# Kernel optimization log

Measured on AMD Instinct MI355X. Metric: run time of the kernel, lower is better.

Reference implementation:

```python
import jax, jax.numpy as jnp
import numpy as np

N_NODES = 30000
N_EDGES = 480000
N_GRAPHS = 128
CONV_PARAMS = [[32, 32], [32, 32], [64, 64], [64, 64], [128, 128], [128, 128]]
IN_FEAT = 5
NUM_CENTROID = 100
NUM_CLASS = 2
BN_EPS = 1e-5


def setup_inputs() -> dict:
    key = jax.random.key(0)
    ks = jax.random.split(key, 64)
    inp = {}
    inp['features'] = jax.random.normal(ks[0], (N_NODES, IN_FEAT), jnp.float32)
    inp['src'] = jax.random.randint(ks[1], (N_EDGES,), 0, N_NODES, jnp.int32)
    inp['dst'] = jax.random.randint(ks[2], (N_EDGES,), 0, N_NODES, jnp.int32)
    inp['graph_id'] = jnp.sort(jax.random.randint(ks[3], (N_NODES,), 0, N_GRAPHS, jnp.int32))
    inp['bn_gamma'] = jnp.ones((IN_FEAT,), jnp.float32)
    inp['bn_beta'] = jnp.zeros((IN_FEAT,), jnp.float32)
    in_f = IN_FEAT
    ki = 4
    for i, (c1, c2) in enumerate(CONV_PARAMS):
        # EdgeConv MLP operates on concat([x_i, x_j - x_i]) -> 2*in_f inputs
        s1 = 1.0 / np.sqrt(2 * in_f)
        s2 = 1.0 / np.sqrt(c1)
        inp[f'W1_{i}'] = jax.random.normal(ks[ki], (2 * in_f, c1), jnp.float32) * s1
        inp[f'b1_{i}'] = jnp.zeros((c1,), jnp.float32)
        inp[f'W2_{i}'] = jax.random.normal(ks[ki + 1], (c1, c2), jnp.float32) * s2
        inp[f'b2_{i}'] = jnp.zeros((c2,), jnp.float32)
        ki += 2
        in_f = c2
    inp['centroids'] = jax.random.normal(ks[ki], (NUM_CENTROID, CONV_PARAMS[-1][-1]), jnp.float32)
    inp['fc_w'] = jax.random.normal(ks[ki + 1], (NUM_CENTROID, NUM_CLASS), jnp.float32) * (1.0 / np.sqrt(NUM_CENTROID))
    inp['fc_b'] = jnp.zeros((NUM_CLASS,), jnp.float32)
    return inp


def _edge_conv(x, src, dst, deg_inv, W1, b1, W2, b2):
    # DGCNN-style EdgeConv: MLP([x_i, x_j - x_i]) then mean-aggregate to dst node
    xi = x[dst]                                   # [E, F]
    xj = x[src]                                   # [E, F]
    e = jnp.concatenate([xi, xj - xi], axis=-1)   # [E, 2F]
    h = jax.nn.relu(e @ W1 + b1)
    h = jax.nn.relu(h @ W2 + b2)
    return jax.ops.segment_sum(h, dst, num_segments=x.shape[0]) * deg_inv


def reference(features, src, dst, graph_id, bn_gamma, bn_beta,
              W1_0, b1_0, W2_0, b2_0, W1_1, b1_1, W2_1, b2_1,
              W1_2, b1_2, W2_2, b2_2, W1_3, b1_3, W2_3, b2_3,
              W1_4, b1_4, W2_4, b2_4, W1_5, b1_5, W2_5, b2_5,
              centroids, fc_w, fc_b):
    N = features.shape[0]
    # BatchNorm1d in training mode (batch statistics over nodes)
    mu = features.mean(axis=0)
    var = features.var(axis=0)
    x = (features - mu) / jnp.sqrt(var + BN_EPS) * bn_gamma + bn_beta

    # in-degree for mean aggregation
    deg = jax.ops.segment_sum(jnp.ones_like(dst, jnp.float32), dst, num_segments=N)
    deg_inv = (1.0 / jnp.maximum(deg, 1.0))[:, None]

    params = [(W1_0, b1_0, W2_0, b2_0), (W1_1, b1_1, W2_1, b2_1),
              (W1_2, b1_2, W2_2, b2_2), (W1_3, b1_3, W2_3, b2_3),
              (W1_4, b1_4, W2_4, b2_4), (W1_5, b1_5, W2_5, b2_5)]
    for W1, b1, W2, b2 in params:
        x = _edge_conv(x, src, dst, deg_inv, W1, b1, W2, b2)  # [N, c2]

    # CentroidDistance (Euclidean manifold): dist of each node to each centroid
    diff = x[:, None, :] - centroids[None, :, :]              # [N, C, D]
    dist = jnp.sqrt(jnp.sum(diff * diff, axis=-1) + 1e-12)    # [N, C]

    # per-graph mean pooling of centroid distances
    cnt = jax.ops.segment_sum(jnp.ones((N,), jnp.float32), graph_id, num_segments=N_GRAPHS)
    pooled = jax.ops.segment_sum(dist, graph_id, num_segments=N_GRAPHS) / jnp.maximum(cnt, 1.0)[:, None]

    return pooled @ fc_w + fc_b  # [G, num_class]
```

## Files before the change

kernel.cpp:

```cpp
#include <hip/hip_runtime.h>
#include <hip/hip_fp16.h>

#define N_NODES 30000
#define N_EDGES 480000
#define N_GRAPHS 128
#define IN_FEAT 5
#define NUM_CENTROID 100
#define BN_EPS 1e-5f

typedef unsigned int u32;
typedef unsigned short u16;

using half8 = __attribute__((ext_vector_type(8))) _Float16;
using h2    = __attribute__((ext_vector_type(2))) _Float16;
using f32x4 = __attribute__((ext_vector_type(4))) float;

__device__ __forceinline__ u16 f2h(float x) {
    return __half_as_ushort(__float2half_rn(x));
}
__device__ __forceinline__ float h2f(u16 h) {
    return __half2float(__ushort_as_half(h));
}
__device__ __forceinline__ u32 pack2h(float lo, float hi) {
    return (u32)f2h(lo) | ((u32)f2h(hi) << 16);
}

#define BN_BLKS 118
#define DSTH_BLKS 1875
__global__ __launch_bounds__(256) void setup1_kernel(
    const float* __restrict__ f, float* __restrict__ acc,
    const int* __restrict__ dst, int* __restrict__ counts)
{
    const int b = blockIdx.x;
    if (b < BN_BLKS) {
        int n = b * 256 + threadIdx.x;
        float q[10];
        #pragma unroll
        for (int k = 0; k < 10; ++k) q[k] = 0.f;
        if (n < N_NODES) {
            #pragma unroll
            for (int k = 0; k < IN_FEAT; ++k) {
                float v = f[n * IN_FEAT + k];
                q[k] = v;
                q[5 + k] = v * v;
            }
        }
        #pragma unroll
        for (int k = 0; k < 10; ++k) {
            #pragma unroll
            for (int o = 32; o > 0; o >>= 1)
                q[k] += __shfl_xor(q[k], o);
        }
        if ((threadIdx.x & 63) == 0) {
            #pragma unroll
            for (int k = 0; k < 10; ++k) atomicAdd(&acc[k], q[k]);
        }
    } else {
        int e = (b - BN_BLKS) * 256 + threadIdx.x;
        if (e < N_EDGES) atomicAdd(&counts[dst[e]], 1);
    }
}

__global__ __launch_bounds__(1024) void scan_kernel(
    const int* __restrict__ counts, int* __restrict__ row_off,
    float* __restrict__ deg_inv, int N)
{
    __shared__ int s[1024];
    const int CH = 30;
    int t = threadIdx.x;
    int base = t * CH;
    int loc = 0;
    for (int j = 0; j < CH; ++j) {
        int i = base + j;
        if (i < N) loc += counts[i];
    }
    s[t] = loc;
    __syncthreads();
    for (int off = 1; off < 1024; off <<= 1) {
        int v = (t >= off) ? s[t - off] : 0;
        __syncthreads();
        s[t] += v;
        __syncthreads();
    }
    int run = s[t] - loc;
    for (int j = 0; j < CH; ++j) {
        int i = base + j;
        if (i < N) {
            int cv = counts[i];
            row_off[i] = run;
            run += cv;
            deg_inv[i] = 1.0f / fmaxf((float)cv, 1.0f);
        }
    }
    if (t == 1023) row_off[N] = s[1023];
}

__constant__ __device__ const int LFIN[6] = {5, 32, 32, 64, 64, 128};
__constant__ __device__ const int LKD[6]  = {32, 32, 32, 64, 64, 128};
__constant__ __device__ const int LCD[6]  = {32, 32, 64, 64, 128, 128};
__constant__ __device__ const int W1OFF[6] = {0, 2048, 4096, 8192, 16384, 32768};
__constant__ __device__ const int W2OFF[6] = {0, 1024, 2048, 6144, 10240, 26624};
#define W1TOT 65536
#define W2TOT 43008
#define CTOT  14336
#define PREP_TOT (W1TOT + W2TOT + CTOT + 112)

#define CSR_BLKS 1875
#define BNN_BLKS 586

struct Setup2Args {
    const int* dst; const int* src; const int* row_off; int* cursor;
    int* csr_src; int* csr_dst;
    const float* f; const float* acc; const float* gamma; const float* beta;
    float* X0;
    const float* w1[6]; const float* w2[6]; const float* cent;
    u16* w1img; u16* w2img; u16* centimg; float* csq;
};

__global__ __launch_bounds__(256) void setup2_kernel(Setup2Args a)
{
    const int b = blockIdx.x;
    if (b < CSR_BLKS) {
        int e = b * 256 + threadIdx.x;
        if (e < N_EDGES) {
            int d = a.dst[e];
            int p = atomicAdd(&a.cursor[d], 1);
            a.csr_src[a.row_off[d] + p] = a.src[e];
            a.csr_dst[a.row_off[d] + p] = d;
        }
        return;
    }
    if (b < CSR_BLKS + BNN_BLKS) {
        int i = (b - CSR_BLKS) * 256 + threadIdx.x;
        if (i < N_NODES * IN_FEAT) {
            int k = i % IN_FEAT;
            float mu = a.acc[k] / (float)N_NODES;
            float var = a.acc[5 + k] / (float)N_NODES - mu * mu;
            float sc = a.gamma[k] / sqrtf(var + BN_EPS);
            a.X0[i] = (a.f[i] - mu) * sc + a.beta[k];
        }
        return;
    }
    int gid = (b - CSR_BLKS - BNN_BLKS) * 256 + threadIdx.x;
    if (gid < W1TOT) {
        int l = 0;
        #pragma unroll
        for (int i = 1; i < 6; ++i) if (gid >= W1OFF[i]) l = i;
        int local = gid - W1OFF[l];
        int K = LKD[l], C = LCD[l], F = LFIN[l];
        int n = local / K, k = local % K;
        float v = 0.f;
        if (k < F) {
            if (n < C) v = a.w1[l][k * C + n] - a.w1[l][(F + k) * C + n];
            else       v = a.w1[l][(F + k) * C + (n - C)];
        }
        int byte = (local * 2) ^ ((n & 7) << 4);
        *(u16*)((char*)a.w1img + (size_t)W1OFF[l] * 2 + byte) = f2h(v);
        return;
    }
    int g2 = gid - W1TOT;
    if (g2 < W2TOT) {
        int l = 0;
        #pragma unroll
        for (int i = 1; i < 6; ++i) if (g2 >= W2OFF[i]) l = i;
        int local = g2 - W2OFF[l];
        int C = LCD[l];
        int n = local / C, k = local % C;
        float v = a.w2[l][k * C + n];
        int byte = (local * 2) ^ ((n & 7) << 4);
        *(u16*)((char*)a.w2img + (size_t)W2OFF[l] * 2 + byte) = f2h(v);
        return;
    }
    int g3 = g2 - W2TOT;
    if (g3 < CTOT) {
        int c = g3 / 128, d = g3 % 128;
        float v = (c < NUM_CENTROID) ? a.cent[c * 128 + d] : 0.f;
        int byte = (g3 * 2) ^ ((c & 7) << 4);
        *(u16*)((char*)a.centimg + byte) = f2h(v);
        return;
    }
    int c = g3 - CTOT;
    if (c < 112) {
        float s = 0.f;
        if (c < NUM_CENTROID) {
            for (int d = 0; d < 128; ++d) {
                float cv = h2f(f2h(a.cent[c * 128 + d]));
                s += cv * cv;
            }
        }
        a.csq[c] = s;
    }
}

template <int FIN, int K, int C>
__global__ __launch_bounds__(256) void node_mfma_kernel(
    const float* __restrict__ Xin, const float* __restrict__ scale,
    const u16* __restrict__ w1img, const float* __restrict__ b1,
    u16* __restrict__ U, u16* __restrict__ V, int N)
{
    constexpr int COLS = 2 * C;
    __shared__ u16 wt[COLS * K];
    __shared__ u16 xt[32 * K];

    for (int i = threadIdx.x; i < COLS * K / 8; i += 256)
        reinterpret_cast<uint4*>(wt)[i] = reinterpret_cast<const uint4*>(w1img)[i];

    constexpr int DPT = K / 8;
    const int nl = threadIdx.x >> 3;
    const int part = threadIdx.x & 7;
    const int n = blockIdx.x * 32 + nl;
    const int k0 = part * DPT;
    const bool vld = (n < N);
    float s = 1.f;
    if (vld && scale) s = scale[n];

    float xv[DPT];
    if constexpr (FIN == K) {
        #pragma unroll
        for (int j4 = 0; j4 < DPT / 4; ++j4) {
            float4 f4 = {0, 0, 0, 0};
            if (vld) f4 = *reinterpret_cast<const float4*>(Xin + (size_t)n * FIN + k0 + j4 * 4);
            xv[j4 * 4 + 0] = f4.x * s; xv[j4 * 4 + 1] = f4.y * s;
            xv[j4 * 4 + 2] = f4.z * s; xv[j4 * 4 + 3] = f4.w * s;
        }
    } else {
        #pragma unroll
        for (int j = 0; j < DPT; ++j) {
            int k = k0 + j;
            xv[j] = (vld && k < FIN) ? Xin[(size_t)n * FIN + k] * s : 0.f;
        }
    }

    if constexpr (DPT == 4) {
        u32 o[2];
        o[0] = pack2h(xv[0], xv[1]);
        o[1] = pack2h(xv[2], xv[3]);
        int byte = ((nl * K + k0) * 2) ^ ((nl & 7) << 4);
        *reinterpret_cast<uint2*>((char*)xt + byte) = *reinterpret_cast<uint2*>(o);
    } else {
        #pragma unroll
        for (int j8 = 0; j8 < DPT / 8; ++j8) {
            u32 o[4];
            #pragma unroll
            for (int q = 0; q < 4; ++q)
                o[q] = pack2h(xv[j8 * 8 + q * 2], xv[j8 * 8 + q * 2 + 1]);
            int byte = ((nl * K + k0 + j8 * 8) * 2) ^ ((nl & 7) << 4);
            *reinterpret_cast<uint4*>((char*)xt + byte) = *reinterpret_cast<uint4*>(o);
        }
    }
    __syncthreads();

    constexpr int NT = COLS / 16;
    constexpr int NPW = NT / 4;
    constexpr int KS = K / 32;

    const int wid = threadIdx.x >> 6;
    const int lane = threadIdx.x & 63;
    const int lrow = lane & 15;
    const int lk8 = (lane >> 4) * 8;

    f32x4 acc[2][NPW] = {};

    #pragma unroll
    for (int ks = 0; ks < KS; ++ks) {
        half8 afrag[2];
        #pragma unroll
        for (int m = 0; m < 2; ++m) {
            int row = m * 16 + lrow;
            int byte = ((row * K + ks * 32 + lk8) * 2) ^ ((row & 7) << 4);
            afrag[m] = *reinterpret_cast<const half8*>((const char*)xt + byte);
        }
        #pragma unroll
        for (int nn = 0; nn < NPW; ++nn) {
            int colr = (wid * NPW + nn) * 16 + lrow;
            int byte = ((colr * K + ks * 32 + lk8) * 2) ^ ((colr & 7) << 4);
            half8 bfrag = *reinterpret_cast<const half8*>((const char*)wt + byte);
            #pragma unroll
            for (int m = 0; m < 2; ++m)
                acc[m][nn] = __builtin_amdgcn_mfma_f32_16x16x32_f16(
                    afrag[m], bfrag, acc[m][nn], 0, 0, 0);
        }
    }

    #pragma unroll
    for (int nn = 0; nn < NPW; ++nn) {
        int colr = (wid * NPW + nn) * 16 + lrow;
        float bias = (colr < C) ? b1[colr] : 0.f;
        #pragma unroll
        for (int m = 0; m < 2; ++m) {
            #pragma unroll
            for (int j = 0; j < 4; ++j) {
                int row = m * 16 + (lane >> 4) * 4 + j;
                int node = blockIdx.x * 32 + row;
                if (node < N) {
                    float z = acc[m][nn][j] + bias;
                    if (colr < C) U[(size_t)node * C + colr] = f2h(z);
                    else          V[(size_t)node * C + colr - C] = f2h(z);
                }
            }
        }
    }
}

template <int C, int ET>
__global__ __launch_bounds__(256, 4) void edge_agg_kernel(
    const u16* __restrict__ U, const u16* __restrict__ V,
    const int* __restrict__ csr_src, const int* __restrict__ csr_dst,
    const u16* __restrict__ w2img, const float* __restrict__ b2,
    float* __restrict__ Xout, int E)
{
    constexpr int PAD = 2;
    __shared__ u16 at[ET * (C + PAD)];
    __shared__ int dstid[ET];

    constexpr int MT = ET / 16;
    constexpr int NT = C / 16;
    constexpr int WN = (NT < 4) ? NT : 4;
    constexpr int WM = 4 / WN;
    constexpr int MPW = MT / WM;
    constexpr int NPW = NT / WN;
    constexpr int KS = C / 32;

    const int wid = threadIdx.x >> 6;
    const int lane = threadIdx.x & 63;
    const int wn = wid % WN;
    const int wm = wid / WN;
    const int lrow = lane & 15;
    const int lk8 = (lane >> 4) * 8;

    half8 bfrag[NPW][KS];
    #pragma unroll
    for (int n = 0; n < NPW; ++n) {
        int col = (wn * NPW + n) * 16 + lrow;
        #pragma unroll
        for (int ks = 0; ks < KS; ++ks) {
            int byte = ((col * C + ks * 32 + lk8) * 2) ^ ((col & 7) << 4);
            bfrag[n][ks] = *reinterpret_cast<const half8*>((const char*)w2img + byte);
        }
    }

    constexpr int TPE = 256 / ET;
    const int e_loc = threadIdx.x / TPE;
    const int part  = threadIdx.x % TPE;
    const int k0 = part * 32;
    const int e = blockIdx.x * ET + e_loc;
    const bool valid = (e < E);
    const int dn = valid ? csr_dst[e] : 0;
    const int sn = valid ? csr_src[e] : 0;
    if (part == 0) dstid[e_loc] = valid ? dn : -1;

    const h2 zz = {(_Float16)0.f, (_Float16)0.f};
    const u16* Ur = U + (size_t)dn * C + k0;
    const u16* Vr = V + (size_t)sn * C + k0;
    #pragma unroll
    for (int j = 0; j < 4; ++j) {
        uint4 uu = {0, 0, 0, 0}, vv = {0, 0, 0, 0};
        if (valid) {
            uu = *reinterpret_cast<const uint4*>(Ur + j * 8);
            vv = *reinterpret_cast<const uint4*>(Vr + j * 8);
        }
        h2 o[4];
        const h2* ua = reinterpret_cast<const h2*>(&uu);
        const h2* va = reinterpret_cast<const h2*>(&vv);
        #pragma unroll
        for (int q = 0; q < 4; ++q)
            o[q] = __builtin_elementwise_max(ua[q] + va[q], zz);
        int byte = ((e_loc * C + k0 + j * 8) * 2) ^ ((e_loc & 7) << 4);
        *reinterpret_cast<uint4*>((char*)at + byte) = *reinterpret_cast<const uint4*>(o);
    }
    __syncthreads();

    f32x4 acc[MPW][NPW] = {};

    #pragma unroll
    for (int ks = 0; ks < KS; ++ks) {
        half8 afrag[MPW];
        #pragma unroll
        for (int m = 0; m < MPW; ++m) {
            int row = (wm * MPW + m) * 16 + lrow;
            int byte = ((row * C + ks * 32 + lk8) * 2) ^ ((row & 7) << 4);
            afrag[m] = *reinterpret_cast<const half8*>((const char*)at + byte);
        }
        #pragma unroll
        for (int m = 0; m < MPW; ++m)
            #pragma unroll
            for (int n = 0; n < NPW; ++n)
                acc[m][n] = __builtin_amdgcn_mfma_f32_16x16x32_f16(
                    afrag[m], bfrag[n][ks], acc[m][n], 0, 0, 0);
    }
    __syncthreads();

    #pragma unroll
    for (int m = 0; m < MPW; ++m) {
        #pragma unroll
        for (int n = 0; n < NPW; ++n) {
            int col = (wn * NPW + n) * 16 + lrow;
            float bb = b2[col];
            #pragma unroll
            for (int j = 0; j < 4; ++j) {
                int row = (wm * MPW + m) * 16 + (lane >> 4) * 4 + j;
                at[row * (C + PAD) + col] = f2h(fmaxf(acc[m][n][j] + bb, 0.f));
            }
        }
    }
    __syncthreads();

    constexpr int EPS = ET * C / 256;
    const int col = threadIdx.x & (C - 1);
    const int e0 = (threadIdx.x / C) * EPS;
    float sum = 0.f;
    int cur = dstid[e0];
    #pragma unroll 4
    for (int ee = e0; ee < e0 + EPS; ++ee) {
        int d = dstid[ee];
        if (d != cur) {
            if (cur >= 0) atomicAdd(&Xout[(size_t)cur * C + col], sum);
            sum = 0.f;
            cur = d;
        }
        sum += h2f(at[ee * (C + PAD) + col]);
    }
    if (cur >= 0) atomicAdd(&Xout[(size_t)cur * C + col], sum);
}

__global__ __launch_bounds__(256) void dist_pool_kernel(
    const float* __restrict__ X, const float* __restrict__ scale,
    const u16* __restrict__ centimg, const float* __restrict__ csq,
    const int* __restrict__ gid, float* __restrict__ psum, int N)
{
    __shared__ char smem[46784];
    u16* ct = (u16*)smem;
    u16* xt = (u16*)(smem + 28672);
    float* xsqp = (float*)(smem + 45056);
    float* csqs = (float*)(smem + 46080);
    int* gidS   = (int*)(smem + 46528);
    float* dt   = (float*)smem;

    for (int i = threadIdx.x; i < 112 * 128 / 8; i += 256)
        reinterpret_cast<uint4*>(ct)[i] = reinterpret_cast<const uint4*>(centimg)[i];
    if (threadIdx.x < 112) csqs[threadIdx.x] = csq[threadIdx.x];
    if (threadIdx.x < 64) {
        int n = blockIdx.x * 64 + threadIdx.x;
        gidS[threadIdx.x] = (n < N) ? gid[n] : -1;
    }

    const int nl = threadIdx.x >> 2;
    const int part = threadIdx.x & 3;
    const int n = blockIdx.x * 64 + nl;
    const int k0 = part * 32;
    const bool vld = (n < N);
    const float s = vld ? scale[n] : 0.f;

    float ss = 0.f;
    #pragma unroll
    for (int j8 = 0; j8 < 4; ++j8) {
        float4 f0 = {0, 0, 0, 0}, f1 = {0, 0, 0, 0};
        if (vld) {
            f0 = *reinterpret_cast<const float4*>(X + (size_t)n * 128 + k0 + j8 * 8);
            f1 = *reinterpret_cast<const float4*>(X + (size_t)n * 128 + k0 + j8 * 8 + 4);
        }
        float xv[8] = {f0.x * s, f0.y * s, f0.z * s, f0.w * s,
                       f1.x * s, f1.y * s, f1.z * s, f1.w * s};
        u32 o[4];
        #pragma unroll
        for (int q = 0; q < 4; ++q) {
            float lo = h2f(f2h(xv[q * 2]));
            float hi = h2f(f2h(xv[q * 2 + 1]));
            ss += lo * lo + hi * hi;
            o[q] = pack2h(xv[q * 2], xv[q * 2 + 1]);
        }
        int byte = ((nl * 128 + k0 + j8 * 8) * 2) ^ ((nl & 7) << 4);
        *reinterpret_cast<uint4*>((char*)xt + byte) = *reinterpret_cast<uint4*>(o);
    }
    xsqp[nl * 4 + part] = ss;
    __syncthreads();

    const int wid = threadIdx.x >> 6;
    const int lane = threadIdx.x & 63;
    const int lrow = lane & 15;
    const int lk8 = (lane >> 4) * 8;

    f32x4 acc[7] = {};
    #pragma unroll
    for (int ks = 0; ks < 4; ++ks) {
        int row = wid * 16 + lrow;
        int byte = ((row * 128 + ks * 32 + lk8) * 2) ^ ((row & 7) << 4);
        half8 afrag = *reinterpret_cast<const half8*>((const char*)xt + byte);
        #pragma unroll
        for (int nn = 0; nn < 7; ++nn) {
            int colr = nn * 16 + lrow;
            int bb = ((colr * 128 + ks * 32 + lk8) * 2) ^ ((colr & 7) << 4);
            half8 bfrag = *reinterpret_cast<const half8*>((const char*)ct + bb);
            acc[nn] = __builtin_amdgcn_mfma_f32_16x16x32_f16(afrag, bfrag, acc[nn], 0, 0, 0);
        }
    }

    float xs[4];
    #pragma unroll
    for (int j = 0; j < 4; ++j) {
        int row = wid * 16 + (lane >> 4) * 4 + j;
        xs[j] = xsqp[row * 4 + 0] + xsqp[row * 4 + 1] + xsqp[row * 4 + 2] + xsqp[row * 4 + 3];
    }
    __syncthreads();

    #pragma unroll
    for (int nn = 0; nn < 7; ++nn) {
        int colr = nn * 16 + lrow;
        float cq = csqs[colr];
        #pragma unroll
        for (int j = 0; j < 4; ++j) {
            int row = wid * 16 + (lane >> 4) * 4 + j;
            float v = xs[j] - 2.f * acc[nn][j] + cq;
            dt[row * 112 + colr] = sqrtf(fmaxf(v, 0.f) + 1e-12f);
        }
    }
    __syncthreads();

    if (threadIdx.x < 200) {
        const int col = threadIdx.x % 100;
        const int r0 = (threadIdx.x / 100) * 32;
        float sum = 0.f;
        int cur = gidS[r0];
        for (int r = r0; r < r0 + 32; ++r) {
            int g = gidS[r];
            if (g != cur) {
                if (cur >= 0) atomicAdd(&psum[cur * NUM_CENTROID + col], sum);
                sum = 0.f;
                cur = g;
            }
            if (g >= 0) sum += dt[r * 112 + col];
        }
        if (cur >= 0) atomicAdd(&psum[cur * NUM_CENTROID + col], sum);
    }
}

__global__ __launch_bounds__(256) void fc_kernel(
    const float* __restrict__ psum, const int* __restrict__ gid,
    const float* __restrict__ fc_w, const float* __restrict__ fc_b,
    float* __restrict__ out, int N)
{
    const int g = threadIdx.x >> 1;
    const int cls = threadIdx.x & 1;
    int lo = 0, hi = N;
    while (lo < hi) { int mid = (lo + hi) >> 1; if (gid[mid] < g) lo = mid + 1; else hi = mid; }
    const int start = lo;
    hi = N;
    while (lo < hi) { int mid = (lo + hi) >> 1; if (gid[mid] < g + 1) lo = mid + 1; else hi = mid; }
    float cnt = fmaxf((float)(lo - start), 1.0f);
    float o = 0.f;
    for (int c = 0; c < NUM_CENTROID; ++c)
        o += psum[g * NUM_CENTROID + c] * fc_w[c * 2 + cls];
    out[g * 2 + cls] = fc_b[cls] + o / cnt;
}

static const int W1OFF_H[6] = {0, 2048, 4096, 8192, 16384, 32768};
static const int W2OFF_H[6] = {0, 1024, 2048, 6144, 10240, 26624};

extern "C" void kernel_launch(void* const* d_in, const int* in_sizes, int n_in,
                              void* d_out, int out_size, void* d_ws, size_t ws_size,
                              hipStream_t stream) {
    const float* features = (const float*)d_in[0];
    const int*   src      = (const int*)d_in[1];
    const int*   dst      = (const int*)d_in[2];
    const int*   gid      = (const int*)d_in[3];
    const float* gamma    = (const float*)d_in[4];
    const float* beta     = (const float*)d_in[5];
    const float *W1[6], *b1[6], *W2[6], *b2[6];
    for (int i = 0; i < 6; ++i) {
        W1[i] = (const float*)d_in[6 + 4 * i];
        b1[i] = (const float*)d_in[7 + 4 * i];
        W2[i] = (const float*)d_in[8 + 4 * i];
        b2[i] = (const float*)d_in[9 + 4 * i];
    }
    const float* centroids = (const float*)d_in[30];
    const float* fc_w      = (const float*)d_in[31];
    const float* fc_b      = (const float*)d_in[32];

    const int N = N_NODES, E = N_EDGES;

    char* p = (char*)d_ws;
    size_t off = 0;
    auto alloc = [&](size_t bytes) {
        void* r = p + off;
        off += (bytes + 255) & ~(size_t)255;
        return r;
    };

    float* X0bn = (float*)alloc((size_t)N * IN_FEAT * 4);
    char* xz0 = p + off;
    float* XL[6];
    const int LCC[6] = {32, 32, 64, 64, 128, 128};
    for (int i = 0; i < 6; ++i) XL[i] = (float*)alloc((size_t)N * LCC[i] * 4);
    size_t xzbytes = (size_t)((p + off) - xz0);

    u16* Uh = (u16*)alloc((size_t)N * 128 * 2);
    u16* Vh = (u16*)alloc((size_t)N * 128 * 2);

    int*   row_off = (int*)alloc((size_t)(N + 1) * 4);
    int*   csr_src = (int*)alloc((size_t)E * 4);
    int*   csr_dst = (int*)alloc((size_t)E * 4);
    float* deg_inv = (float*)alloc((size_t)N * 4);
    u16*   w1img   = (u16*)alloc((size_t)W1TOT * 2);
    u16*   w2img   = (u16*)alloc((size_t)W2TOT * 2);
    u16*   centimg = (u16*)alloc((size_t)CTOT * 2);
    float* csq     = (float*)alloc(112 * 4);

    char*  zero0   = (char*)(p + off);
    int*   counts  = (int*)alloc((size_t)N * 4);
    int*   cursor  = (int*)alloc((size_t)N * 4);
    float* bnacc   = (float*)alloc(64);
    float* psum    = (float*)alloc((size_t)N_GRAPHS * NUM_CENTROID * 4);
    size_t zbytes  = (size_t)((char*)(p + off) - zero0);

    (void)hipMemsetAsync(xz0, 0, xzbytes, stream);
    (void)hipMemsetAsync(zero0, 0, zbytes, stream);

    setup1_kernel<<<BN_BLKS + DSTH_BLKS, 256, 0, stream>>>(
        features, bnacc, dst, counts);
    scan_kernel<<<1, 1024, 0, stream>>>(counts, row_off, deg_inv, N);

    Setup2Args sa;
    sa.dst = dst; sa.src = src; sa.row_off = row_off; sa.cursor = cursor;
    sa.csr_src = csr_src; sa.csr_dst = csr_dst;
    sa.f = features; sa.acc = bnacc; sa.gamma = gamma; sa.beta = beta; sa.X0 = X0bn;
    for (int i = 0; i < 6; ++i) { sa.w1[i] = W1[i]; sa.w2[i] = W2[i]; }
    sa.cent = centroids; sa.w1img = w1img; sa.w2img = w2img;
    sa.centimg = centimg; sa.csq = csq;
    const int S2B = CSR_BLKS + BNN_BLKS + (PREP_TOT + 255) / 256;
    setup2_kernel<<<S2B, 256, 0, stream>>>(sa);

    const int NB = (N + 31) / 32;

    node_mfma_kernel<5, 32, 32><<<NB, 256, 0, stream>>>(
        X0bn, (const float*)nullptr, w1img + W1OFF_H[0], b1[0], Uh, Vh, N);
    edge_agg_kernel<32, 256><<<(E + 255) / 256, 256, 0, stream>>>(
        Uh, Vh, csr_src, csr_dst, w2img + W2OFF_H[0], b2[0], XL[0], E);

    node_mfma_kernel<32, 32, 32><<<NB, 256, 0, stream>>>(
        XL[0], deg_inv, w1img + W1OFF_H[1], b1[1], Uh, Vh, N);
    edge_agg_kernel<32, 256><<<(E + 255) / 256, 256, 0, stream>>>(
        Uh, Vh, csr_src, csr_dst, w2img + W2OFF_H[1], b2[1], XL[1], E);

    node_mfma_kernel<32, 32, 64><<<NB, 256, 0, stream>>>(
        XL[1], deg_inv, w1img + W1OFF_H[2], b1[2], Uh, Vh, N);
    edge_agg_kernel<64, 128><<<(E + 127) / 128, 256, 0, stream>>>(
        Uh, Vh, csr_src, csr_dst, w2img + W2OFF_H[2], b2[2], XL[2], E);

    node_mfma_kernel<64, 64, 64><<<NB, 256, 0, stream>>>(
        XL[2], deg_inv, w1img + W1OFF_H[3], b1[3], Uh, Vh, N);
    edge_agg_kernel<64, 128><<<(E + 127) / 128, 256, 0, stream>>>(
        Uh, Vh, csr_src, csr_dst, w2img + W2OFF_H[3], b2[3], XL[3], E);

    node_mfma_kernel<64, 64, 128><<<NB, 256, 0, stream>>>(
        XL[3], deg_inv, w1img + W1OFF_H[4], b1[4], Uh, Vh, N);
    edge_agg_kernel<128, 64><<<(E + 63) / 64, 256, 0, stream>>>(
        Uh, Vh, csr_src, csr_dst, w2img + W2OFF_H[4], b2[4], XL[4], E);

    node_mfma_kernel<128, 128, 128><<<NB, 256, 0, stream>>>(
        XL[4], deg_inv, w1img + W1OFF_H[5], b1[5], Uh, Vh, N);
    edge_agg_kernel<128, 64><<<(E + 63) / 64, 256, 0, stream>>>(
        Uh, Vh, csr_src, csr_dst, w2img + W2OFF_H[5], b2[5], XL[5], E);

    dist_pool_kernel<<<(N + 63) / 64, 256, 0, stream>>>(
        XL[5], deg_inv, centimg, csq, gid, psum, N);
    fc_kernel<<<1, 256, 0, stream>>>(psum, gid, fc_w, fc_b, (float*)d_out, N);
}
```

Baseline: 548.3 us.

## Build CSR with chunked LDS histograms and zero outputs in node kernels

Replaces the global-atomic degree count and cursor-based CSR fill with per-chunk shared-memory histograms plus a column prefix over chunks, so each edge's slot is computed deterministically without global atomics. It also drops the large up-front memset of per-layer output buffers: layers ping-pong between two buffers, and each node kernel zeroes the next layer's output rows. This adds extra kernels and a sizable partial-count array (60×N ints) and rank array, and relies on the zeroing completing before the edge kernel accumulates.

Result: faster. 533.2 us (-2.8%).

```diff
diff --git a/kernel.cpp b/kernel.cpp
--- a/kernel.cpp
+++ b/kernel.cpp
@@ -25,15 +25,36 @@
     return (u32)f2h(lo) | ((u32)f2h(hi) << 16);
 }
 
-#define BN_BLKS 118
-#define DSTH_BLKS 1875
-__global__ __launch_bounds__(256) void setup1_kernel(
-    const float* __restrict__ f, float* __restrict__ acc,
-    const int* __restrict__ dst, int* __restrict__ counts)
+#define HCHUNKS 60
+#define EPC 8000
+#define HIST_BLKS 120
+#define BN1_BLKS 30
+
+__global__ __launch_bounds__(1024) void hist_kernel(
+    const int* __restrict__ dst, int* __restrict__ rank_local,
+    int* __restrict__ partial,
+    const float* __restrict__ f, float* __restrict__ acc)
 {
     const int b = blockIdx.x;
-    if (b < BN_BLKS) {
-        int n = b * 256 + threadIdx.x;
+    if (b < HIST_BLKS) {
+        __shared__ int lh[15000];
+        const int chunk = b >> 1;
+        const int nbase = (b & 1) * 15000;
+        for (int i = threadIdx.x; i < 15000; i += 1024) lh[i] = 0;
+        __syncthreads();
+        const int e0 = chunk * EPC;
+        for (int e = e0 + threadIdx.x; e < e0 + EPC; e += 1024) {
+            int dl = dst[e] - nbase;
+            if (dl >= 0 && dl < 15000) {
+                int r = atomicAdd(&lh[dl], 1);
+                rank_local[e] = r;
+            }
+        }
+        __syncthreads();
+        for (int i = threadIdx.x; i < 15000; i += 1024)
+            partial[chunk * N_NODES + nbase + i] = lh[i];
+    } else {
+        int n = (b - HIST_BLKS) * 1024 + threadIdx.x;
         float q[10];
         #pragma unroll
         for (int k = 0; k < 10; ++k) q[k] = 0.f;
@@ -55,9 +76,38 @@
             #pragma unroll
             for (int k = 0; k < 10; ++k) atomicAdd(&acc[k], q[k]);
         }
+    }
+}
+
+#define COLSUM_BLKS 118
+#define BNN_BLKS 586
+__global__ __launch_bounds__(256) void colsum_kernel(
+    int* __restrict__ partial, int* __restrict__ counts,
+    const float* __restrict__ f, const float* __restrict__ acc,
+    const float* __restrict__ gamma, const float* __restrict__ beta,
+    float* __restrict__ X0)
+{
+    const int b = blockIdx.x;
+    if (b < COLSUM_BLKS) {
+        int n = b * 256 + threadIdx.x;
+        if (n < N_NODES) {
+            int run = 0;
+            for (int c = 0; c < HCHUNKS; ++c) {
+                int v = partial[c * N_NODES + n];
+                partial[c * N_NODES + n] = run;
+                run += v;
+            }
+            counts[n] = run;
+        }
     } else {
-        int e = (b - BN_BLKS) * 256 + threadIdx.x;
-        if (e < N_EDGES) atomicAdd(&counts[dst[e]], 1);
+        int i = (b - COLSUM_BLKS) * 256 + threadIdx.x;
+        if (i < N_NODES * IN_FEAT) {
+            int k = i % IN_FEAT;
+            float mu = acc[k] / (float)N_NODES;
+            float var = acc[5 + k] / (float)N_NODES - mu * mu;
+            float sc = gamma[k] / sqrtf(var + BN_EPS);
+            X0[i] = (f[i] - mu) * sc + beta[k];
+        }
     }
 }
 
@@ -104,44 +154,30 @@
 #define W2TOT 43008
 #define CTOT  14336
 #define PREP_TOT (W1TOT + W2TOT + CTOT + 112)
-
 #define CSR_BLKS 1875
-#define BNN_BLKS 586
-
-struct Setup2Args {
-    const int* dst; const int* src; const int* row_off; int* cursor;
+
+struct FillArgs {
+    const int* dst; const int* src; const int* row_off;
+    const int* rank_local; const int* partial;
     int* csr_src; int* csr_dst;
-    const float* f; const float* acc; const float* gamma; const float* beta;
-    float* X0;
     const float* w1[6]; const float* w2[6]; const float* cent;
     u16* w1img; u16* w2img; u16* centimg; float* csq;
 };
 
-__global__ __launch_bounds__(256) void setup2_kernel(Setup2Args a)
+__global__ __launch_bounds__(256) void fill_kernel(FillArgs a)
 {
     const int b = blockIdx.x;
     if (b < CSR_BLKS) {
         int e = b * 256 + threadIdx.x;
         if (e < N_EDGES) {
             int d = a.dst[e];
-            int p = atomicAdd(&a.cursor[d], 1);
-            a.csr_src[a.row_off[d] + p] = a.src[e];
-            a.csr_dst[a.row_off[d] + p] = d;
+            int slot = a.row_off[d] + a.partial[(e / EPC) * N_NODES + d] + a.rank_local[e];
+            a.csr_src[slot] = a.src[e];
+            a.csr_dst[slot] = d;
         }
         return;
     }
-    if (b < CSR_BLKS + BNN_BLKS) {
-        int i = (b - CSR_BLKS) * 256 + threadIdx.x;
-        if (i < N_NODES * IN_FEAT) {
-            int k = i % IN_FEAT;
-            float mu = a.acc[k] / (float)N_NODES;
-            float var = a.acc[5 + k] / (float)N_NODES - mu * mu;
-            float sc = a.gamma[k] / sqrtf(var + BN_EPS);
-            a.X0[i] = (a.f[i] - mu) * sc + a.beta[k];
-        }
-        return;
-    }
-    int gid = (b - CSR_BLKS - BNN_BLKS) * 256 + threadIdx.x;
+    int gid = (b - CSR_BLKS) * 256 + threadIdx.x;
     if (gid < W1TOT) {
         int l = 0;
         #pragma unroll
@@ -192,11 +228,12 @@
     }
 }
 
-template <int FIN, int K, int C>
+template <int FIN, int K, int C, int CZ>
 __global__ __launch_bounds__(256) void node_mfma_kernel(
     const float* __restrict__ Xin, const float* __restrict__ scale,
     const u16* __restrict__ w1img, const float* __restrict__ b1,
-    u16* __restrict__ U, u16* __restrict__ V, int N)
+    u16* __restrict__ U, u16* __restrict__ V,
+    float* __restrict__ Xzero, int N)
 {
     constexpr int COLS = 2 * C;
     __shared__ u16 wt[COLS * K];
@@ -246,6 +283,17 @@
                 o[q] = pack2h(xv[j8 * 8 + q * 2], xv[j8 * 8 + q * 2 + 1]);
             int byte = ((nl * K + k0 + j8 * 8) * 2) ^ ((nl & 7) << 4);
             *reinterpret_cast<uint4*>((char*)xt + byte) = *reinterpret_cast<uint4*>(o);
+        }
+    }
+
+    if constexpr (CZ > 0) {
+        constexpr int V4 = CZ / 4;
+        const float4 z4 = {0.f, 0.f, 0.f, 0.f};
+        for (int i = threadIdx.x; i < 32 * V4; i += 256) {
+            int row = i / V4, c4 = i % V4;
+            int nz = blockIdx.x * 32 + row;
+            if (nz < N)
+                reinterpret_cast<float4*>(Xzero + (size_t)nz * CZ)[c4] = z4;
         }
     }
     __syncthreads();
@@ -587,81 +635,78 @@
     };
 
     float* X0bn = (float*)alloc((size_t)N * IN_FEAT * 4);
-    char* xz0 = p + off;
-    float* XL[6];
-    const int LCC[6] = {32, 32, 64, 64, 128, 128};
-    for (int i = 0; i < 6; ++i) XL[i] = (float*)alloc((size_t)N * LCC[i] * 4);
-    size_t xzbytes = (size_t)((p + off) - xz0);
-
-    u16* Uh = (u16*)alloc((size_t)N * 128 * 2);
-    u16* Vh = (u16*)alloc((size_t)N * 128 * 2);
-
-    int*   row_off = (int*)alloc((size_t)(N + 1) * 4);
-    int*   csr_src = (int*)alloc((size_t)E * 4);
-    int*   csr_dst = (int*)alloc((size_t)E * 4);
-    float* deg_inv = (float*)alloc((size_t)N * 4);
-    u16*   w1img   = (u16*)alloc((size_t)W1TOT * 2);
-    u16*   w2img   = (u16*)alloc((size_t)W2TOT * 2);
-    u16*   centimg = (u16*)alloc((size_t)CTOT * 2);
-    float* csq     = (float*)alloc(112 * 4);
-
-    char*  zero0   = (char*)(p + off);
-    int*   counts  = (int*)alloc((size_t)N * 4);
-    int*   cursor  = (int*)alloc((size_t)N * 4);
-    float* bnacc   = (float*)alloc(64);
-    float* psum    = (float*)alloc((size_t)N_GRAPHS * NUM_CENTROID * 4);
-    size_t zbytes  = (size_t)((char*)(p + off) - zero0);
-
-    (void)hipMemsetAsync(xz0, 0, xzbytes, stream);
+    float* XA   = (float*)alloc((size_t)N * 128 * 4);
+    float* XB   = (float*)alloc((size_t)N * 128 * 4);
+    u16*   Uh   = (u16*)alloc((size_t)N * 128 * 2);
+    u16*   Vh   = (u16*)alloc((size_t)N * 128 * 2);
+
+    int*   row_off    = (int*)alloc((size_t)(N + 1) * 4);
+    int*   csr_src    = (int*)alloc((size_t)E * 4);
+    int*   csr_dst    = (int*)alloc((size_t)E * 4);
+    float* deg_inv    = (float*)alloc((size_t)N * 4);
+    int*   counts     = (int*)alloc((size_t)N * 4);
+    int*   rank_local = (int*)alloc((size_t)E * 4);
+    int*   partial    = (int*)alloc((size_t)HCHUNKS * N * 4);
+    u16*   w1img      = (u16*)alloc((size_t)W1TOT * 2);
+    u16*   w2img      = (u16*)alloc((size_t)W2TOT * 2);
+    u16*   centimg    = (u16*)alloc((size_t)CTOT * 2);
+    float* csq        = (float*)alloc(112 * 4);
+
+    char*  zero0 = (char*)(p + off);
+    float* bnacc = (float*)alloc(64);
+    float* psum  = (float*)alloc((size_t)N_GRAPHS * NUM_CENTROID * 4);
+    size_t zbytes = (size_t)((char*)(p + off) - zero0);
+
     (void)hipMemsetAsync(zero0, 0, zbytes, stream);
 
-    setup1_kernel<<<BN_BLKS + DSTH_BLKS, 256, 0, stream>>>(
-        features, bnacc, dst, counts);
+    hist_kernel<<<HIST_BLKS + BN1_BLKS, 1024, 0, stream>>>(
+        dst, rank_local, partial, features, bnacc);
+    colsum_kernel<<<COLSUM_BLKS + BNN_BLKS, 256, 0, stream>>>(
+        partial, counts, features, bnacc, gamma, beta, X0bn);
     scan_kernel<<<1, 1024, 0, stream>>>(counts, row_off, deg_inv, N);
 
-    Setup2Args sa;
-    sa.dst = dst; sa.src = src; sa.row_off = row_off; sa.cursor = cursor;
-    sa.csr_src = csr_src; sa.csr_dst = csr_dst;
-    sa.f = features; sa.acc = bnacc; sa.gamma = gamma; sa.beta = beta; sa.X0 = X0bn;
-    for (int i = 0; i < 6; ++i) { sa.w1[i] = W1[i]; sa.w2[i] = W2[i]; }
-    sa.cent = centroids; sa.w1img = w1img; sa.w2img = w2img;
-    sa.centimg = centimg; sa.csq = csq;
-    const int S2B = CSR_BLKS + BNN_BLKS + (PREP_TOT + 255) / 256;
-    setup2_kernel<<<S2B, 256, 0, stream>>>(sa);
+    FillArgs fa;
+    fa.dst = dst; fa.src = src; fa.row_off = row_off;
+    fa.rank_local = rank_local; fa.partial = partial;
+    fa.csr_src = csr_src; fa.csr_dst = csr_dst;
+    for (int i = 0; i < 6; ++i) { fa.w1[i] = W1[i]; fa.w2[i] = W2[i]; }
+    fa.cent = centroids; fa.w1img = w1img; fa.w2img = w2img;
+    fa.centimg = centimg; fa.csq = csq;
+    fill_kernel<<<CSR_BLKS + (PREP_TOT + 255) / 256, 256, 0, stream>>>(fa);
 
     const int NB = (N + 31) / 32;
 
-    node_mfma_kernel<5, 32, 32><<<NB, 256, 0, stream>>>(
-        X0bn, (const float*)nullptr, w1img + W1OFF_H[0], b1[0], Uh, Vh, N);
+    node_mfma_kernel<5, 32, 32, 32><<<NB, 256, 0, stream>>>(
+        X0bn, (const float*)nullptr, w1img + W1OFF_H[0], b1[0], Uh, Vh, XA, N);
     edge_agg_kernel<32, 256><<<(E + 255) / 256, 256, 0, stream>>>(
-        Uh, Vh, csr_src, csr_dst, w2img + W2OFF_H[0], b2[0], XL[0], E);
-
-    node_mfma_kernel<32, 32, 32><<<NB, 256, 0, stream>>>(
-        XL[0], deg_inv, w1img + W1OFF_H[1], b1[1], Uh, Vh, N);
+        Uh, Vh, csr_src, csr_dst, w2img + W2OFF_H[0], b2[0], XA, E);
+
+    node_mfma_kernel<32, 32, 32, 32><<<NB, 256, 0, stream>>>(
+        XA, deg_inv, w1img + W1OFF_H[1], b1[1], Uh, Vh, XB, N);
     edge_agg_kernel<32, 256><<<(E + 255) / 256, 256, 0, stream>>>(
-        Uh, Vh, csr_src, csr_dst, w2img + W2OFF_H[1], b2[1], XL[1], E);
-
-    node_mfma_kernel<32, 32, 64><<<NB, 256, 0, stream>>>(
-        XL[1], deg_inv, w1img + W1OFF_H[2], b1[2], Uh, Vh, N);
+        Uh, Vh, csr_src, csr_dst, w2img + W2OFF_H[1], b2[1], XB, E);
+
+    node_mfma_kernel<32, 32, 64, 64><<<NB, 256, 0, stream>>>(
+        XB, deg_inv, w1img + W1OFF_H[2], b1[2], Uh, Vh, XA, N);
     edge_agg_kernel<64, 128><<<(E + 127) / 128, 256, 0, stream>>>(
-        Uh, Vh, csr_src, csr_dst, w2img + W2OFF_H[2], b2[2], XL[2], E);
-
-    node_mfma_kernel<64, 64, 64><<<NB, 256, 0, stream>>>(
-        XL[2], deg_inv, w1img + W1OFF_H[3], b1[3], Uh, Vh, N);
+        Uh, Vh, csr_src, csr_dst, w2img + W2OFF_H[2], b2[2], XA, E);
+
+    node_mfma_kernel<64, 64, 64, 64><<<NB, 256, 0, stream>>>(
+        XA, deg_inv, w1img + W1OFF_H[3], b1[3], Uh, Vh, XB, N);
     edge_agg_kernel<64, 128><<<(E + 127) / 128, 256, 0, stream>>>(
-        Uh, Vh, csr_src, csr_dst, w2img + W2OFF_H[3], b2[3], XL[3], E);
-
-    node_mfma_kernel<64, 64, 128><<<NB, 256, 0, stream>>>(
-        XL[3], deg_inv, w1img + W1OFF_H[4], b1[4], Uh, Vh, N);
+        Uh, Vh, csr_src, csr_dst, w2img + W2OFF_H[3], b2[3], XB, E);
+
+    node_mfma_kernel<64, 64, 128, 128><<<NB, 256, 0, stream>>>(
+        XB, deg_inv, w1img + W1OFF_H[4], b1[4], Uh, Vh, XA, N);
     edge_agg_kernel<128, 64><<<(E + 63) / 64, 256, 0, stream>>>(
-        Uh, Vh, csr_src, csr_dst, w2img + W2OFF_H[4], b2[4], XL[4], E);
-
-    node_mfma_kernel<128, 128, 128><<<NB, 256, 0, stream>>>(
-        XL[4], deg_inv, w1img + W1OFF_H[5], b1[5], Uh, Vh, N);
+        Uh, Vh, csr_src, csr_dst, w2img + W2OFF_H[4], b2[4], XA, E);
+
+    node_mfma_kernel<128, 128, 128, 128><<<NB, 256, 0, stream>>>(
+        XA, deg_inv, w1img + W1OFF_H[5], b1[5], Uh, Vh, XB, N);
     edge_agg_kernel<128, 64><<<(E + 63) / 64, 256, 0, stream>>>(
-        Uh, Vh, csr_src, csr_dst, w2img + W2OFF_H[5], b2[5], XL[5], E);
+        Uh, Vh, csr_src, csr_dst, w2img + W2OFF_H[5], b2[5], XB, E);
 
     dist_pool_kernel<<<(N + 63) / 64, 256, 0, stream>>>(
-        XL[5], deg_inv, centimg, csq, gid, psum, N);
+        XB, deg_inv, centimg, csq, gid, psum, N);
     fc_kernel<<<1, 256, 0, stream>>>(psum, gid, fc_w, fc_b, (float*)d_out, N);
 }
```
